# Performance work log

Hardware: AMD Instinct MI355X
Metric: run time of the kernel (lower is better)

The kernel has to match this reference:

```python
import jax, jax.numpy as jnp
import numpy as np

NPOINT, NSAMPLE, RADIUS = 2048, 32, 0.2
EPS = 1e-5


def setup_inputs() -> dict:
    key = jax.random.key(0)
    ks = jax.random.split(key, 12)
    B, N, C = 8, 8192, 64
    mlp = [64, 64, 128]
    inp = {
        "xyz": jax.random.normal(ks[0], (B, 3, N), dtype=jnp.float32),
        "points": jax.random.normal(ks[1], (B, C, N), dtype=jnp.float32),
    }
    last = C + 3  # use_xyz concatenates 3 relative coords
    for i, out in enumerate(mlp, 1):
        inp[f"W{i}"] = jax.random.normal(ks[2 * i], (out, last), dtype=jnp.float32) / np.sqrt(last).astype(np.float32)
        inp[f"b{i}"] = jnp.zeros((out,), jnp.float32)
        inp[f"g{i}"] = jnp.ones((out,), jnp.float32)
        inp[f"be{i}"] = jnp.zeros((out,), jnp.float32)
        last = out
    return inp


def fps(xyz_t, npoint):
    """Farthest point sampling. xyz_t: (B,N,3) -> (B,npoint) int32 indices."""
    xyz_t = jax.lax.stop_gradient(xyz_t)  # indices are non-differentiable
    B, N, _ = xyz_t.shape

    def step(carry, _):
        dists, far = carry  # (B,N), (B,)
        cent = jnp.take_along_axis(xyz_t, far[:, None, None], axis=1)  # (B,1,3)
        d = jnp.sum((xyz_t - cent) ** 2, axis=-1)
        dists = jnp.minimum(dists, d)
        nf = jnp.argmax(dists, axis=-1).astype(jnp.int32)
        return (dists, nf), far

    init = (jnp.full((B, N), 1e10, xyz_t.dtype), jnp.zeros((B,), jnp.int32))
    _, idxs = jax.lax.scan(step, init, None, length=npoint)
    return jnp.transpose(idxs)  # (B, npoint)


def ball_query(xyz_t, new_xyz_t, radius, nsample):
    """First-nsample-in-radius neighbor indices, padded with first hit.
    xyz_t (B,N,3), new_xyz_t (B,M,3) -> (B,M,nsample) int32."""
    B, N, _ = xyz_t.shape
    # squared distances via gemm to avoid (B,M,N,3) intermediate
    sq = (jnp.sum(new_xyz_t ** 2, -1)[:, :, None]
          + jnp.sum(xyz_t ** 2, -1)[:, None, :]
          - 2.0 * jnp.einsum('bmd,bnd->bmn', new_xyz_t, xyz_t))  # (B,M,N)
    cand = jnp.where(sq < radius * radius, jnp.arange(N, dtype=jnp.int32), N)
    idx = jnp.sort(cand, axis=-1)[:, :, :nsample]  # first k in-radius by index order
    first = idx[:, :, :1]
    first = jnp.where(first == N, 0, first)  # guard empty groups
    idx = jnp.where(idx == N, first, idx)
    return idx


def group(feat, idx):
    """feat (B,C,N), idx (B,M,k) -> (B,C,M,k) gathered neighbor features."""
    return jnp.take_along_axis(feat[:, :, None, :], idx[:, None, :, :], axis=3)


def conv_bn_relu(x, W, b, g, be):
    """Shared 1x1 Conv2d + BatchNorm2d (batch stats, training mode) + ReLU.
    x: (B,C,M,K) -> (B,O,M,K)."""
    y = jnp.einsum('oc,bcmk->bomk', W, x) + b[None, :, None, None]
    mu = jnp.mean(y, axis=(0, 2, 3), keepdims=True)
    var = jnp.var(y, axis=(0, 2, 3), keepdims=True)
    y = (y - mu) * jax.lax.rsqrt(var + EPS)
    y = y * g[None, :, None, None] + be[None, :, None, None]
    return jax.nn.relu(y)


def reference(xyz, points, W1, b1, g1, be1, W2, b2, g2, be2, W3, b3, g3, be3):
    xyz_t = jnp.transpose(xyz, (0, 2, 1))  # (B,N,3)
    fidx = fps(xyz_t, NPOINT)  # (B,M)
    new_xyz = jnp.take_along_axis(xyz, fidx[:, None, :], axis=2)  # (B,3,M)
    idx = ball_query(xyz_t, jnp.transpose(new_xyz, (0, 2, 1)), RADIUS, NSAMPLE)  # (B,M,K)
    grouped_xyz = group(xyz, idx) - new_xyz[:, :, :, None]  # (B,3,M,K) centered
    grouped_pts = group(points, idx)  # (B,f,M,K)
    x = jnp.concatenate([grouped_xyz, grouped_pts], axis=1)  # (B,f+3,M,K)
    x = conv_bn_relu(x, W1, b1, g1, be1)
    x = conv_bn_relu(x, W2, b2, g2, be2)
    x = conv_bn_relu(x, W3, b3, g3, be3)
    new_points = jnp.max(x, axis=3)  # (B,mlp[-1],M)
    return (new_xyz, new_points)
```

## Files before the change

### kernel.cpp

```cpp
#include <hip/hip_runtime.h>

#define BB 8
#define NN 8192
#define MM 2048
#define KK 32
#define NTOT (BB*MM*KK)

#define WS_PTS_T  0
#define WS_XYZN   4194304
#define WS_IDX    5242880
#define WS_GPART  5767168
#define WS_PARAMS 6291456
#define WS_ZMAX   6292480
#define WS_ZMIN   8389632
#define WS_TOTAL  10486784

typedef float v2f __attribute__((ext_vector_type(2)));

__global__ __launch_bounds__(256) void k_transpose(const float* __restrict__ pts,
                                                   float* __restrict__ pts_t){
  __shared__ float tile[64][65];
  int bid = blockIdx.x;
  int b = bid >> 7;
  int n0 = (bid & 127) << 6;
  int tx = threadIdx.x & 63, ty = threadIdx.x >> 6;
  const float* src = pts + (size_t)b*64*NN;
  #pragma unroll
  for (int c = ty; c < 64; c += 4)
    tile[c][tx] = src[(size_t)c*NN + n0 + tx];
  __syncthreads();
  float* dst = pts_t + ((size_t)b*NN + n0)*64;
  #pragma unroll
  for (int r = ty; r < 64; r += 4)
    dst[(size_t)r*64 + tx] = tile[tx][r];
}

__global__ __launch_bounds__(256) void k_xyzn(const float* __restrict__ xyz,
                                              float4* __restrict__ xyzn){
  #pragma clang fp contract(off)
  int i = blockIdx.x*256 + threadIdx.x;
  int b = i >> 13, n = i & 8191;
  const float* p = xyz + (size_t)b*3*NN;
  float x = p[n], y = p[NN+n], z = p[2*NN+n];
  float nrm = (x*x + y*y) + z*z;
  xyzn[i] = make_float4(x, y, z, nrm);
}

#define DPPMAXF(ctrl, rmask)                                                 \
  {                                                                          \
    float s_ = __int_as_float(__builtin_amdgcn_update_dpp(                   \
        __float_as_int(m), __float_as_int(m), (ctrl), (rmask), 0xf, false)); \
    m = fmaxf(m, s_);                                                        \
  }

__global__ __launch_bounds__(256,1) void k_fps(const float* __restrict__ xyz,
                                               float* __restrict__ out_newxyz){
  #pragma clang fp contract(off)
  __shared__ float4 sp4[NN];
  __shared__ unsigned long long swk[2][4];
  int b = blockIdx.x, tid = threadIdx.x;
  const float* xb = xyz + (size_t)b*3*NN;
  int n0 = tid << 5;
  v2f px[16], py[16], pz[16], dd[16];
  const float4* xb4 = (const float4*)xb;
  #pragma unroll
  for (int q = 0; q < 8; ++q){
    float4 X = xb4[(n0>>2) + q];
    float4 Y = xb4[(NN>>2) + (n0>>2) + q];
    float4 Z = xb4[((2*NN)>>2) + (n0>>2) + q];
    px[2*q]   = (v2f){X.x, X.y}; px[2*q+1] = (v2f){X.z, X.w};
    py[2*q]   = (v2f){Y.x, Y.y}; py[2*q+1] = (v2f){Y.z, Y.w};
    pz[2*q]   = (v2f){Z.x, Z.y}; pz[2*q+1] = (v2f){Z.z, Z.w};
    dd[2*q]   = (v2f){1e10f,1e10f}; dd[2*q+1] = (v2f){1e10f,1e10f};
    sp4[n0+4*q+0] = make_float4(X.x, Y.x, Z.x, 0.f);
    sp4[n0+4*q+1] = make_float4(X.y, Y.y, Z.y, 0.f);
    sp4[n0+4*q+2] = make_float4(X.z, Y.z, Z.z, 0.f);
    sp4[n0+4*q+3] = make_float4(X.w, Y.w, Z.w, 0.f);
  }
  __syncthreads();
  float4 c0 = sp4[0];
  float cx = c0.x, cy = c0.y, cz = c0.z;
  float* ob = out_newxyz + (size_t)b*3*MM;
  int lane = tid & 63, wid = tid >> 6;
  for (int s = 0; s < 8; ++s){
    float ox = 0.f, oy = 0.f, oz = 0.f;
    #pragma unroll 1
    for (int ti = 0; ti < 256; ++ti){
      if (tid == ti){ ox = cx; oy = cy; oz = cz; }
      v2f cvx = (v2f){cx,cx}, cvy = (v2f){cy,cy}, cvz = (v2f){cz,cz};
      v2f bv2 = (v2f){-1.f,-1.f};
      #pragma unroll
      for (int g = 0; g < 16; ++g){
        v2f dx = px[g]-cvx, dy = py[g]-cvy, dz = pz[g]-cvz;
        v2f xx = dx*dx, yy = dy*dy, zz = dz*dz;
        v2f sm = xx + yy;
        v2f d  = sm + zz;
        v2f nd = __builtin_elementwise_min(dd[g], d);
        dd[g] = nd;
        bv2 = __builtin_elementwise_max(bv2, nd);
      }
      float bv = fmaxf(bv2.x, bv2.y);
      float m = bv;
      DPPMAXF(0x111, 0xf)
      DPPMAXF(0x112, 0xf)
      DPPMAXF(0x114, 0xf)
      DPPMAXF(0x118, 0xf)
      DPPMAXF(0x142, 0xa)
      DPPMAXF(0x143, 0xc)
      float wm = __int_as_float(__builtin_amdgcn_readlane(__float_as_int(m), 63));
      unsigned long long msk = __ballot(bv == wm);
      int wl = (int)__builtin_ctzll(msk);
      int bj = 0;
      #pragma unroll
      for (int g = 15; g >= 0; --g){
        if (dd[g].y == bv) bj = 2*g+1;
        if (dd[g].x == bv) bj = 2*g;
      }
      int nwin = __builtin_amdgcn_readlane(n0 + bj, wl);
      int buf = ti & 1;
      if (lane == 0){
        unsigned long long key =
            ((unsigned long long)__float_as_uint(wm) << 32) |
            (unsigned int)(~(unsigned int)nwin);
        swk[buf][wid] = key;
      }
      __syncthreads();
      const unsigned long long* kk = swk[buf];
      unsigned long long k0=kk[0], k1=kk[1], k2=kk[2], k3=kk[3];
      unsigned long long a = (k0>k1)?k0:k1, c2 = (k2>k3)?k2:k3;
      unsigned long long kmax = (a>c2)?a:c2;
      int far = (int)(~(unsigned int)kmax) & (NN-1);
      float4 c4 = sp4[far];
      cx = c4.x; cy = c4.y; cz = c4.z;
    }
    ob[(s<<8)+tid] = ox; ob[MM+(s<<8)+tid] = oy; ob[2*MM+(s<<8)+tid] = oz;
  }
}

__global__ __launch_bounds__(256) void k_ballq(const float4* __restrict__ xyzn,
                                               const float* __restrict__ newxyz,
                                               int* __restrict__ idx){
  #pragma clang fp contract(off)
  __shared__ unsigned long long s_mask[32][129];
  __shared__ float4 s_c4[32];
  const float R2 = (float)(0.2*0.2);
  int b = blockIdx.x >> 6;
  int m0 = (blockIdx.x & 63) << 5;
  int tid = threadIdx.x, lane = tid & 63, wv = tid >> 6;
  const float* nb = newxyz + (size_t)b*3*MM;
  if (tid < 32){
    int m = m0 + tid;
    float cx = nb[m], cy = nb[MM+m], cz = nb[2*MM+m];
    float cn = (cx*cx + cy*cy) + cz*cz;
    s_c4[tid] = make_float4(cx, cy, cz, cn);
  }
  __syncthreads();
  const float4* src = xyzn + (size_t)b*NN;
  for (int ci = 0; ci < 32; ++ci){
    int ch = ci*4 + wv;
    float4 p = src[ch*64 + lane];
    #pragma unroll 8
    for (int mi = 0; mi < 32; ++mi){
      float4 c = s_c4[mi];
      float dot = (c.x*p.x + c.y*p.y) + c.z*p.z;
      float sq = (c.w + p.w) - 2.0f*dot;
      unsigned long long mk = __ballot(sq < R2);
      if (lane == 0) s_mask[mi][ch] = mk;
    }
  }
  __syncthreads();
  if (tid < 32){
    int m = m0 + tid;
    int* om = idx + ((size_t)(b*MM + m))*KK;
    int filled = 0, first = -1;
    for (int ch = 0; ch < 128 && filled < KK; ++ch){
      unsigned long long mk = s_mask[tid][ch];
      while (mk){
        int bp = __builtin_ctzll(mk);
        mk &= mk - 1;
        int j = ch*64 + bp;
        if (first < 0) first = j;
        om[filled++] = j;
        if (filled == KK) break;
      }
    }
    int pad = (first < 0) ? 0 : first;
    for (int s = filled; s < KK; ++s) om[s] = pad;
  }
}

#define XST 260
#define PSTW 130

__device__ __forceinline__ void gemm_step(v2f (&acc)[8][2], const float* sw,
                                          const float* sx, int c, int ob8, int pb){
  float4 X = *(const float4*)&sx[c*XST + pb];
  v2f x0 = (v2f){X.x, X.y}, x1 = (v2f){X.z, X.w};
  float4 W0 = *(const float4*)&sw[c*64 + ob8];
  float4 W1 = *(const float4*)&sw[c*64 + ob8 + 4];
  float ws[8] = {W0.x,W0.y,W0.z,W0.w,W1.x,W1.y,W1.z,W1.w};
  #pragma unroll
  for (int oi = 0; oi < 8; ++oi){
    v2f wv = (v2f){ws[oi], ws[oi]};
    acc[oi][0] = __builtin_elementwise_fma(wv, x0, acc[oi][0]);
    acc[oi][1] = __builtin_elementwise_fma(wv, x1, acc[oi][1]);
  }
}

__device__ __forceinline__ void zero_acc(v2f (&acc)[8][2]){
  #pragma unroll
  for (int oi = 0; oi < 8; ++oi){ acc[oi][0] = (v2f){0.f,0.f}; acc[oi][1] = (v2f){0.f,0.f}; }
}

__device__ __forceinline__ void gather_col(float* sx, const float* pts_t,
    const float4* xyzn, const float* nb, const int* idx, int b, int bid, int tid){
  int pos = tid & 255, half = tid >> 8;
  int m0 = (bid & 255) << 3;
  int m = m0 + (pos >> 5), k = pos & 31;
  int j = idx[((size_t)(b*MM + m))*KK + k];
  const float4* pf = (const float4*)(pts_t + ((size_t)b*NN + j)*64);
  if (half == 0){
    float4 P = xyzn[(size_t)b*NN + j];
    sx[0*XST + pos] = P.x - nb[m];
    sx[1*XST + pos] = P.y - nb[MM+m];
    sx[2*XST + pos] = P.z - nb[2*MM+m];
    #pragma unroll
    for (int c4 = 0; c4 < 8; ++c4){
      float4 v = pf[c4];
      sx[(3+4*c4+0)*XST + pos] = v.x;
      sx[(3+4*c4+1)*XST + pos] = v.y;
      sx[(3+4*c4+2)*XST + pos] = v.z;
      sx[(3+4*c4+3)*XST + pos] = v.w;
    }
  } else {
    #pragma unroll
    for (int c4 = 8; c4 < 16; ++c4){
      float4 v = pf[c4];
      sx[(3+4*c4+0)*XST + pos] = v.x;
      sx[(3+4*c4+1)*XST + pos] = v.y;
      sx[(3+4*c4+2)*XST + pos] = v.z;
      sx[(3+4*c4+3)*XST + pos] = v.w;
    }
  }
}

__device__ __forceinline__ void bnrelu_tile(v2f (&acc)[8][2], const float* sA,
                                            const float* sC, int ob8){
  v2f Z = (v2f){0.f, 0.f};
  #pragma unroll
  for (int oi = 0; oi < 8; ++oi){
    v2f Av = (v2f){sA[ob8+oi], sA[ob8+oi]};
    v2f Cv = (v2f){sC[ob8+oi], sC[ob8+oi]};
    acc[oi][0] = __builtin_elementwise_max(__builtin_elementwise_fma(Av, acc[oi][0], Cv), Z);
    acc[oi][1] = __builtin_elementwise_max(__builtin_elementwise_fma(Av, acc[oi][1], Cv), Z);
  }
}

__device__ __forceinline__ void stash_tile(const v2f (&acc)[8][2], float* sx,
                                           int ob8, int pb){
  #pragma unroll
  for (int oi = 0; oi < 8; ++oi)
    *(float4*)&sx[(ob8+oi)*XST + pb] =
        make_float4(acc[oi][0].x, acc[oi][0].y, acc[oi][1].x, acc[oi][1].y);
}

__device__ __forceinline__ void tile_stats(const v2f (&acc)[8][2], float* s_pp,
    float* gpart, int ob8, int pg, int tid, int bid){
  #pragma unroll
  for (int oi = 0; oi < 8; ++oi){
    v2f a0 = acc[oi][0], a1 = acc[oi][1];
    float s  = (a0.x + a0.y) + (a1.x + a1.y);
    float q2 = (a0.x*a0.x + a0.y*a0.y) + (a1.x*a1.x + a1.y*a1.y);
    int o = ob8 + oi;
    s_pp[o*PSTW + pg*2 + 0] = s;
    s_pp[o*PSTW + pg*2 + 1] = q2;
  }
  __syncthreads();
  if (tid < 128){
    int o = tid >> 1, st = tid & 1;
    float S = 0.f;
    #pragma unroll 8
    for (int q = 0; q < 64; ++q) S += s_pp[o*PSTW + q*2 + st];
    gpart[(size_t)(st*128 + o)*2048 + bid] = S;
  }
}

__global__ __launch_bounds__(512,1) void k_conv1_stats(const float* __restrict__ pts_t,
    const float4* __restrict__ xyzn, const float* __restrict__ newxyz,
    const int* __restrict__ idx, const float* __restrict__ W1, float* __restrict__ gpart){
  __shared__ float s_w1[67*64];
  __shared__ float s_x[67*XST];
  int tid = threadIdx.x;
  for (int i = tid; i < 67*64; i += 512){ int c = i>>6, o = i&63; s_w1[i] = W1[o*67 + c]; }
  int bid = blockIdx.x, b = bid >> 8;
  const float* nb = newxyz + (size_t)b*3*MM;
  gather_col(s_x, pts_t, xyzn, nb, idx, b, bid, tid);
  __syncthreads();
  int oq = tid & 7, pg = tid >> 3;
  int ob8 = oq*8, pb = pg*4;
  v2f acc[8][2];
  zero_acc(acc);
  for (int c = 0; c < 67; ++c) gemm_step(acc, s_w1, s_x, c, ob8, pb);
  __syncthreads();
  tile_stats(acc, s_x, gpart, ob8, pg, tid, bid);
}

__global__ __launch_bounds__(512,1) void k_conv2_stats(const float* __restrict__ pts_t,
    const float4* __restrict__ xyzn, const float* __restrict__ newxyz,
    const int* __restrict__ idx, const float* __restrict__ W1, const float* __restrict__ W2,
    const float* __restrict__ params1, float* __restrict__ gpart){
  __shared__ float s_w1[67*64];
  __shared__ float s_w2[64*64];
  __shared__ float s_p[128];
  __shared__ float s_x[67*XST];
  int tid = threadIdx.x;
  for (int i = tid; i < 67*64; i += 512){ int c = i>>6, o = i&63; s_w1[i] = W1[o*67 + c]; }
  for (int i = tid; i < 64*64; i += 512){ int c = i>>6, o = i&63; s_w2[i] = W2[o*64 + c]; }
  if (tid < 64){ s_p[tid] = params1[tid]; s_p[64+tid] = params1[128+tid]; }
  int bid = blockIdx.x, b = bid >> 8;
  const float* nb = newxyz + (size_t)b*3*MM;
  gather_col(s_x, pts_t, xyzn, nb, idx, b, bid, tid);
  __syncthreads();
  int oq = tid & 7, pg = tid >> 3;
  int ob8 = oq*8, pb = pg*4;
  v2f acc[8][2];
  zero_acc(acc);
  for (int c = 0; c < 67; ++c) gemm_step(acc, s_w1, s_x, c, ob8, pb);
  bnrelu_tile(acc, s_p, s_p+64, ob8);
  __syncthreads();
  stash_tile(acc, s_x, ob8, pb);
  __syncthreads();
  zero_acc(acc);
  for (int c = 0; c < 64; ++c) gemm_step(acc, s_w2, s_x, c, ob8, pb);
  __syncthreads();
  tile_stats(acc, s_x, gpart, ob8, pg, tid, bid);
}

__global__ __launch_bounds__(256) void k_bnfin(const float* __restrict__ gpart,
    const float* __restrict__ g, const float* __restrict__ be, float* __restrict__ params){
  int o = blockIdx.x, t = threadIdx.x;
  double s = 0.0, sq = 0.0;
  for (int i = t; i < 2048; i += 256){
    s  += (double)gpart[(size_t)o*2048 + i];
    sq += (double)gpart[(size_t)(128+o)*2048 + i];
  }
  __shared__ double ds[256], dq[256];
  ds[t] = s; dq[t] = sq; __syncthreads();
  for (int off = 128; off > 0; off >>= 1){
    if (t < off){ ds[t] += ds[t+off]; dq[t] += dq[t+off]; }
    __syncthreads();
  }
  if (t == 0){
    double mu = ds[0] / (double)NTOT;
    double var = dq[0] / (double)NTOT - mu*mu;
    float A = g[o] / sqrtf((float)var + 1e-5f);
    float Cc = be[o] - (float)mu * A;
    params[o] = A; params[128+o] = Cc;
  }
}

__global__ __launch_bounds__(512,1) void k_conv3(const float* __restrict__ pts_t,
    const float4* __restrict__ xyzn, const float* __restrict__ newxyz,
    const int* __restrict__ idx, const float* __restrict__ W1, const float* __restrict__ W2,
    const float* __restrict__ W3, const float* __restrict__ params1,
    const float* __restrict__ params2, float* __restrict__ gpart,
    float* __restrict__ zmax, float* __restrict__ zmin){
  __shared__ float s_w1[67*64];
  __shared__ float s_w2[64*64];
  __shared__ float s_w3[64*128];
  __shared__ float s_p[256];
  __shared__ float s_x[67*XST];
  __shared__ float s_sm[8*128*2];
  int tid = threadIdx.x;
  for (int i = tid; i < 67*64; i += 512){ int c = i>>6, o = i&63; s_w1[i] = W1[o*67 + c]; }
  for (int i = tid; i < 64*64; i += 512){ int c = i>>6, o = i&63; s_w2[i] = W2[o*64 + c]; }
  for (int i = tid; i < 64*128; i += 512){ int c = i>>7, o = i&127; s_w3[c*128+o] = W3[o*64 + c]; }
  if (tid < 64){
    s_p[tid]      = params1[tid];     s_p[64+tid]  = params1[128+tid];
    s_p[128+tid]  = params2[tid];     s_p[192+tid] = params2[128+tid];
  }
  int bid = blockIdx.x, b = bid >> 8, m0 = (bid & 255) << 3;
  const float* nb = newxyz + (size_t)b*3*MM;
  gather_col(s_x, pts_t, xyzn, nb, idx, b, bid, tid);
  __syncthreads();
  int oq = tid & 7, pg = tid >> 3;
  int ob8 = oq*8, pb = pg*4;
  v2f acc[8][2];
  zero_acc(acc);
  for (int c = 0; c < 67; ++c) gemm_step(acc, s_w1, s_x, c, ob8, pb);
  bnrelu_tile(acc, s_p, s_p+64, ob8);
  __syncthreads();
  stash_tile(acc, s_x, ob8, pb);
  __syncthreads();
  zero_acc(acc);
  for (int c = 0; c < 64; ++c) gemm_step(acc, s_w2, s_x, c, ob8, pb);
  bnrelu_tile(acc, s_p+128, s_p+192, ob8);
  __syncthreads();
  stash_tile(acc, s_x, ob8, pb);
  __syncthreads();
  int ml = tid >> 6, og = tid & 63;
  v2f accK[2][16];
  #pragma unroll
  for (int oo = 0; oo < 2; ++oo)
    #pragma unroll
    for (int p = 0; p < 16; ++p) accK[oo][p] = (v2f){0.f, 0.f};
  for (int c = 0; c < 64; ++c){
    v2f w = *(const v2f*)&s_w3[c*128 + og*2];
    v2f w0 = (v2f){w.x, w.x}, w1 = (v2f){w.y, w.y};
    #pragma unroll
    for (int q = 0; q < 8; ++q){
      float4 xv = *(const float4*)&s_x[c*XST + ml*32 + q*4];
      v2f xa = (v2f){xv.x, xv.y}, xb2 = (v2f){xv.z, xv.w};
      accK[0][2*q]   = __builtin_elementwise_fma(w0, xa,  accK[0][2*q]);
      accK[0][2*q+1] = __builtin_elementwise_fma(w0, xb2, accK[0][2*q+1]);
      accK[1][2*q]   = __builtin_elementwise_fma(w1, xa,  accK[1][2*q]);
      accK[1][2*q+1] = __builtin_elementwise_fma(w1, xb2, accK[1][2*q+1]);
    }
  }
  int m = m0 + ml;
  #pragma unroll
  for (int oo = 0; oo < 2; ++oo){
    float mx = -3.4e38f, mn = 3.4e38f, s = 0.f, sq = 0.f;
    #pragma unroll
    for (int p = 0; p < 16; ++p){
      float v0 = accK[oo][p].x, v1 = accK[oo][p].y;
      mx = fmaxf(mx, v0); mx = fmaxf(mx, v1);
      mn = fminf(mn, v0); mn = fminf(mn, v1);
      s += v0; s += v1;
      sq = fmaf(v0, v0, sq); sq = fmaf(v1, v1, sq);
    }
    int o = og*2 + oo;
    zmax[((size_t)(b*128 + o))*MM + m] = mx;
    zmin[((size_t)(b*128 + o))*MM + m] = mn;
    s_sm[(ml*128+o)*2] = s; s_sm[(ml*128+o)*2+1] = sq;
  }
  __syncthreads();
  if (tid < 256){
    int o = tid >> 1, st = tid & 1;
    float S = 0.f;
    #pragma unroll
    for (int mm = 0; mm < 8; ++mm) S += s_sm[(mm*128+o)*2 + st];
    gpart[(size_t)(st*128+o)*2048 + bid] = S;
  }
}

__global__ __launch_bounds__(256) void k_out(const float* __restrict__ zmax,
    const float* __restrict__ zmin, const float* __restrict__ params3,
    float* __restrict__ out){
  int i = blockIdx.x*256 + threadIdx.x;
  int o = (i >> 11) & 127;
  float A = params3[o], Cc = params3[128+o];
  float v = (A >= 0.f) ? fmaf(A, zmax[i], Cc) : fmaf(A, zmin[i], Cc);
  out[49152 + i] = fmaxf(v, 0.f);
}

extern "C" void kernel_launch(void* const* d_in, const int* in_sizes, int n_in,
                              void* d_out, int out_size, void* d_ws, size_t ws_size,
                              hipStream_t stream){
  const float* xyz    = (const float*)d_in[0];
  const float* points = (const float*)d_in[1];
  const float* W1  = (const float*)d_in[2];
  const float* g1  = (const float*)d_in[4];
  const float* be1 = (const float*)d_in[5];
  const float* W2  = (const float*)d_in[6];
  const float* g2  = (const float*)d_in[8];
  const float* be2 = (const float*)d_in[9];
  const float* W3  = (const float*)d_in[10];
  const float* g3  = (const float*)d_in[12];
  const float* be3 = (const float*)d_in[13];

  if (ws_size < (size_t)WS_TOTAL * sizeof(float)) return;

  float*  ws     = (float*)d_ws;
  float*  pts_t  = ws + WS_PTS_T;
  float4* xyzn   = (float4*)(ws + WS_XYZN);
  int*    idx    = (int*)(ws + WS_IDX);
  float*  gpart  = ws + WS_GPART;
  float*  params = ws + WS_PARAMS;
  float*  zmax   = ws + WS_ZMAX;
  float*  zmin   = ws + WS_ZMIN;
  float*  out    = (float*)d_out;
  float*  newxyz = out;

  hipLaunchKernelGGL(k_fps,       dim3(8),    dim3(256), 0, stream, xyz, newxyz);
  hipLaunchKernelGGL(k_transpose, dim3(1024), dim3(256), 0, stream, points, pts_t);
  hipLaunchKernelGGL(k_xyzn,      dim3(256),  dim3(256), 0, stream, xyz, xyzn);
  hipLaunchKernelGGL(k_ballq,     dim3(512),  dim3(256), 0, stream, xyzn, newxyz, idx);
  hipLaunchKernelGGL(k_conv1_stats, dim3(2048), dim3(512), 0, stream,
                     pts_t, xyzn, newxyz, idx, W1, gpart);
  hipLaunchKernelGGL(k_bnfin, dim3(64), dim3(256), 0, stream, gpart, g1, be1, params+0);
  hipLaunchKernelGGL(k_conv2_stats, dim3(2048), dim3(512), 0, stream,
                     pts_t, xyzn, newxyz, idx, W1, W2, params+0, gpart);
  hipLaunchKernelGGL(k_bnfin, dim3(64), dim3(256), 0, stream, gpart, g2, be2, params+256);
  hipLaunchKernelGGL(k_conv3, dim3(2048), dim3(512), 0, stream,
                     pts_t, xyzn, newxyz, idx, W1, W2, W3, params+0, params+256,
                     gpart, zmax, zmin);
  hipLaunchKernelGGL(k_bnfin, dim3(128), dim3(256), 0, stream, gpart, g3, be3, params+512);
  hipLaunchKernelGGL(k_out, dim3(8192), dim3(256), 0, stream, zmax, zmin, params+512, out);
}
```

Measured before the change: 2.568 ms.

## Merge transpose and xyz-norm prep into FPS launch; use packed-add inline asm for distances

Folds the points transpose and xyz-norm kernels into the FPS launch as extra blocks. The serial 8-block FPS launch leaves most CUs idle, so the prep work can run alongside it, and two launches disappear. The FPS distance computation becomes hand-written packed add/mul asm on negated centroids, with the min/max split into scalar ops. The shared buffer grows to 128KB for every block, so the prep blocks are limited to one per CU, and the inline asm may interfere with compiler scheduling.

```diff
diff --git a/kernel.cpp b/kernel.cpp
--- a/kernel.cpp
+++ b/kernel.cpp
@@ -17,33 +17,20 @@
 
 typedef float v2f __attribute__((ext_vector_type(2)));
 
-__global__ __launch_bounds__(256) void k_transpose(const float* __restrict__ pts,
-                                                   float* __restrict__ pts_t){
-  __shared__ float tile[64][65];
-  int bid = blockIdx.x;
-  int b = bid >> 7;
-  int n0 = (bid & 127) << 6;
-  int tx = threadIdx.x & 63, ty = threadIdx.x >> 6;
-  const float* src = pts + (size_t)b*64*NN;
-  #pragma unroll
-  for (int c = ty; c < 64; c += 4)
-    tile[c][tx] = src[(size_t)c*NN + n0 + tx];
-  __syncthreads();
-  float* dst = pts_t + ((size_t)b*NN + n0)*64;
-  #pragma unroll
-  for (int r = ty; r < 64; r += 4)
-    dst[(size_t)r*64 + tx] = tile[tx][r];
-}
-
-__global__ __launch_bounds__(256) void k_xyzn(const float* __restrict__ xyz,
-                                              float4* __restrict__ xyzn){
-  #pragma clang fp contract(off)
-  int i = blockIdx.x*256 + threadIdx.x;
-  int b = i >> 13, n = i & 8191;
-  const float* p = xyz + (size_t)b*3*NN;
-  float x = p[n], y = p[NN+n], z = p[2*NN+n];
-  float nrm = (x*x + y*y) + z*z;
-  xyzn[i] = make_float4(x, y, z, nrm);
+__device__ __forceinline__ v2f dist2_pk(v2f px, v2f py, v2f pz,
+                                        v2f ncx, v2f ncy, v2f ncz){
+  v2f t0, t1;
+  asm("v_pk_add_f32 %0, %2, %5\n\t"
+      "v_pk_mul_f32 %0, %0, %0\n\t"
+      "v_pk_add_f32 %1, %3, %6\n\t"
+      "v_pk_mul_f32 %1, %1, %1\n\t"
+      "v_pk_add_f32 %0, %0, %1\n\t"
+      "v_pk_add_f32 %1, %4, %7\n\t"
+      "v_pk_mul_f32 %1, %1, %1\n\t"
+      "v_pk_add_f32 %0, %0, %1"
+      : "=&v"(t0), "=&v"(t1)
+      : "v"(px), "v"(py), "v"(pz), "v"(ncx), "v"(ncy), "v"(ncz));
+  return t0;
 }
 
 #define DPPMAXF(ctrl, rmask)                                                 \
@@ -53,12 +40,45 @@
     m = fmaxf(m, s_);                                                        \
   }
 
-__global__ __launch_bounds__(256,1) void k_fps(const float* __restrict__ xyz,
-                                               float* __restrict__ out_newxyz){
+__global__ __launch_bounds__(256,1) void k_prep_fps(const float* __restrict__ xyz,
+                                                    const float* __restrict__ pts,
+                                                    float* __restrict__ pts_t,
+                                                    float4* __restrict__ xyzn,
+                                                    float* __restrict__ out_newxyz){
   #pragma clang fp contract(off)
-  __shared__ float4 sp4[NN];
+  __shared__ __align__(16) float smem_f[32768];
   __shared__ unsigned long long swk[2][4];
-  int b = blockIdx.x, tid = threadIdx.x;
+  int bid = blockIdx.x, tid = threadIdx.x;
+
+  if (bid >= 8){
+    if (bid < 8 + 1024){
+      int tb = bid - 8;
+      int b = tb >> 7;
+      int n0 = (tb & 127) << 6;
+      int tx = tid & 63, ty = tid >> 6;
+      float* tile = smem_f;
+      const float* src = pts + (size_t)b*64*NN;
+      #pragma unroll
+      for (int c = ty; c < 64; c += 4)
+        tile[c*65 + tx] = src[(size_t)c*NN + n0 + tx];
+      __syncthreads();
+      float* dst = pts_t + ((size_t)b*NN + n0)*64;
+      #pragma unroll
+      for (int r = ty; r < 64; r += 4)
+        dst[(size_t)r*64 + tx] = tile[tx*65 + r];
+    } else {
+      int i = (bid - 1032)*256 + tid;
+      int b = i >> 13, n = i & 8191;
+      const float* p = xyz + (size_t)b*3*NN;
+      float x = p[n], y = p[NN+n], z = p[2*NN+n];
+      float nrm = (x*x + y*y) + z*z;
+      xyzn[i] = make_float4(x, y, z, nrm);
+    }
+    return;
+  }
+
+  float4* sp4 = (float4*)smem_f;
+  int b = bid;
   const float* xb = xyz + (size_t)b*3*NN;
   int n0 = tid << 5;
   v2f px[16], py[16], pz[16], dd[16];
@@ -87,17 +107,17 @@
     #pragma unroll 1
     for (int ti = 0; ti < 256; ++ti){
       if (tid == ti){ ox = cx; oy = cy; oz = cz; }
-      v2f cvx = (v2f){cx,cx}, cvy = (v2f){cy,cy}, cvz = (v2f){cz,cz};
+      v2f ncx = (v2f){-cx,-cx}, ncy = (v2f){-cy,-cy}, ncz = (v2f){-cz,-cz};
       v2f bv2 = (v2f){-1.f,-1.f};
       #pragma unroll
       for (int g = 0; g < 16; ++g){
-        v2f dx = px[g]-cvx, dy = py[g]-cvy, dz = pz[g]-cvz;
-        v2f xx = dx*dx, yy = dy*dy, zz = dz*dz;
-        v2f sm = xx + yy;
-        v2f d  = sm + zz;
-        v2f nd = __builtin_elementwise_min(dd[g], d);
+        v2f d = dist2_pk(px[g], py[g], pz[g], ncx, ncy, ncz);
+        v2f nd;
+        nd.x = fminf(dd[g].x, d.x);
+        nd.y = fminf(dd[g].y, d.y);
         dd[g] = nd;
-        bv2 = __builtin_elementwise_max(bv2, nd);
+        bv2.x = fmaxf(bv2.x, nd.x);
+        bv2.y = fmaxf(bv2.y, nd.y);
       }
       float bv = fmaxf(bv2.x, bv2.y);
       float m = bv;
@@ -482,9 +502,8 @@
   float*  out    = (float*)d_out;
   float*  newxyz = out;
 
-  hipLaunchKernelGGL(k_fps,       dim3(8),    dim3(256), 0, stream, xyz, newxyz);
-  hipLaunchKernelGGL(k_transpose, dim3(1024), dim3(256), 0, stream, points, pts_t);
-  hipLaunchKernelGGL(k_xyzn,      dim3(256),  dim3(256), 0, stream, xyz, xyzn);
+  hipLaunchKernelGGL(k_prep_fps,  dim3(1288), dim3(256), 0, stream,
+                     xyz, points, pts_t, xyzn, newxyz);
   hipLaunchKernelGGL(k_ballq,     dim3(512),  dim3(256), 0, stream, xyzn, newxyz, idx);
   hipLaunchKernelGGL(k_conv1_stats, dim3(2048), dim3(512), 0, stream,
                      pts_t, xyzn, newxyz, idx, W1, gpart);
```

New measurement: 2.662 ms. +3.7%, slower.
